# Kernel tuning notes

Hardware: AMD Instinct MI355X
Metric: run time of the kernel (lower is better)

Reference implementation:

```python
import jax, jax.numpy as jnp
import numpy as np


def setup_inputs() -> dict:
    key = jax.random.key(0)
    ks = jax.random.split(key, 8)
    B, N, C, H = 4, 1024, 512, 8
    return {
        "x": jax.random.normal(ks[0], (B, N, C), jnp.float32),
        "pos": jax.random.normal(ks[1], (B, N, 3), jnp.float32),
        "w_qkv": jax.random.normal(ks[2], (C, 3 * C), jnp.float32) * 0.02,
        "b_qkv": jax.random.normal(ks[3], (3 * C,), jnp.float32) * 0.02,
        "w1": jax.random.normal(ks[4], (3, 64), jnp.float32) * 0.1,
        "b1": jax.random.normal(ks[5], (64,), jnp.float32) * 0.1,
        "w2": jax.random.normal(ks[6], (64, H), jnp.float32) * 0.1,
        "b2": jax.random.normal(ks[7], (H,), jnp.float32) * 0.1,
    }


def reference(x, pos, w_qkv, b_qkv, w1, b1, w2, b2):
    B, N, C = x.shape
    H = w2.shape[1]          # num_heads
    D = C // H               # head_dim
    scale = D ** (-0.5)

    # qkv projection -> q, k, v each [B, H, N, D]
    qkv = (x @ w_qkv + b_qkv).reshape(B, N, 3, H, D)
    qkv = jnp.transpose(qkv, (2, 0, 3, 1, 4))
    q, k, v = qkv[0], qkv[1], qkv[2]

    # pairwise unit direction vectors [B, N, N, 3]
    pos_diff = pos[:, :, None, :] - pos[:, None, :, :]
    pos_norm = jnp.linalg.norm(pos_diff, axis=-1, keepdims=True) + 1e-6
    pos_dir = pos_diff / pos_norm

    # position-MLP bias: [B, N, N, H] -> [B, H, N, N]
    h = jax.nn.relu(pos_dir @ w1 + b1)
    bias = jnp.transpose(h @ w2 + b2, (0, 3, 1, 2))

    attn = jnp.einsum("bhnd,bhmd->bhnm", q, k) * scale + bias
    attn = jax.nn.softmax(attn, axis=-1)
    out = jnp.einsum("bhnm,bhmd->bhnd", attn, v)
    return jnp.transpose(out, (0, 2, 1, 3)).reshape(B, N, C)
```

## Files before the change

kernel.cpp:

```cpp
#include <hip/hip_runtime.h>
#include <hip/hip_bf16.h>
#include <math.h>


typedef __attribute__((ext_vector_type(8))) short bh8;
typedef __attribute__((ext_vector_type(4))) float f32x4;

static __device__ __forceinline__ ushort f2bf(float x) {
    __hip_bfloat16 h = __float2bfloat16(x);
    return *reinterpret_cast<ushort*>(&h);
}
static __device__ __forceinline__ float bf2f(ushort u) {
    unsigned v = ((unsigned)u) << 16;
    return __builtin_bit_cast(float, v);
}

__global__ __launch_bounds__(256) void pos_w1_kernel(
    const float* __restrict__ pos, const float* __restrict__ w1,
    float* __restrict__ apos)
{
    const int idx = blockIdx.x * 256 + threadIdx.x;
    const int bn = idx >> 6, j = idx & 63;
    const float px = pos[bn * 3 + 0];
    const float py = pos[bn * 3 + 1];
    const float pz = pos[bn * 3 + 2];
    apos[idx] = fmaf(px, w1[j], fmaf(py, w1[64 + j], pz * w1[128 + j]));
}

__global__ __launch_bounds__(256) void cast_x_split(
    const float* __restrict__ x, ushort* __restrict__ xh, ushort* __restrict__ xl)
{
    const int idx = blockIdx.x * 256 + threadIdx.x;
    const float4 v = *(const float4*)&x[(size_t)idx * 4];
    ushort h0 = f2bf(v.x), h1 = f2bf(v.y), h2 = f2bf(v.z), h3 = f2bf(v.w);
    ushort l0 = f2bf(v.x - bf2f(h0)), l1 = f2bf(v.y - bf2f(h1));
    ushort l2 = f2bf(v.z - bf2f(h2)), l3 = f2bf(v.w - bf2f(h3));
    uint2 hu, lu;
    hu.x = (unsigned)h0 | ((unsigned)h1 << 16);
    hu.y = (unsigned)h2 | ((unsigned)h3 << 16);
    lu.x = (unsigned)l0 | ((unsigned)l1 << 16);
    lu.y = (unsigned)l2 | ((unsigned)l3 << 16);
    *(uint2*)&xh[(size_t)idx * 4] = hu;
    *(uint2*)&xl[(size_t)idx * 4] = lu;
}

__global__ __launch_bounds__(256) void cast_wT_split(
    const float* __restrict__ w, ushort* __restrict__ wTh, ushort* __restrict__ wTl)
{
    __shared__ float t[64][65];
    const int n0 = blockIdx.x * 64;
    const int k0 = blockIdx.y * 64;
    const int tid = threadIdx.x;
    const int c = tid & 63, r4 = tid >> 6;
#pragma unroll
    for (int i = 0; i < 16; ++i) {
        const int r = i * 4 + r4;
        t[r][c] = w[(size_t)(k0 + r) * 1536 + n0 + c];
    }
    __syncthreads();
#pragma unroll
    for (int i = 0; i < 16; ++i) {
        const int r = i * 4 + r4;
        const float v = t[c][r];
        const ushort hv = f2bf(v);
        wTh[(size_t)(n0 + r) * 512 + k0 + c] = hv;
        wTl[(size_t)(n0 + r) * 512 + k0 + c] = f2bf(v - bf2f(hv));
    }
}

__global__ __launch_bounds__(256, 2) void qkv_mfma(
    const ushort* __restrict__ xh, const ushort* __restrict__ xl,
    const ushort* __restrict__ wTh, const ushort* __restrict__ wTl,
    const float* __restrict__ bqkv,
    ushort* __restrict__ qb, ushort* __restrict__ kb, ushort* __restrict__ vTb)
{
    __shared__ ushort Ah[128 * 68], Al[128 * 68], Bh[128 * 68], Bl[128 * 68];
    const int tid = threadIdx.x;
    const int m0 = blockIdx.x * 128;
    const int n0 = blockIdx.y * 128;
    const int wid = tid >> 6, lane = tid & 63;
    const int wr = wid >> 1, wc = wid & 1;
    const int lq = lane & 15, g = lane >> 4;

    f32x4 acc[4][4];
#pragma unroll
    for (int m = 0; m < 4; ++m)
#pragma unroll
        for (int n = 0; n < 4; ++n) acc[m][n] = (f32x4){0.f, 0.f, 0.f, 0.f};

    const int srow = tid >> 3;
    const int sc8 = (tid & 7) * 8;

    for (int kt = 0; kt < 8; ++kt) {
        const int kk0 = kt * 64;
        __syncthreads();
#pragma unroll
        for (int i = 0; i < 4; ++i) {
            const int row = i * 32 + srow;
            *(bh8*)&Ah[row * 68 + sc8] =
                *(const bh8*)&xh[(size_t)(m0 + row) * 512 + kk0 + sc8];
            *(bh8*)&Al[row * 68 + sc8] =
                *(const bh8*)&xl[(size_t)(m0 + row) * 512 + kk0 + sc8];
            *(bh8*)&Bh[row * 68 + sc8] =
                *(const bh8*)&wTh[(size_t)(n0 + row) * 512 + kk0 + sc8];
            *(bh8*)&Bl[row * 68 + sc8] =
                *(const bh8*)&wTl[(size_t)(n0 + row) * 512 + kk0 + sc8];
        }
        __syncthreads();
#pragma unroll
        for (int kc = 0; kc < 2; ++kc) {
            const int ko = kc * 32 + g * 8;
            bh8 afh[4], afl[4], bfh[4], bfl[4];
#pragma unroll
            for (int m = 0; m < 4; ++m) {
                afh[m] = *(const bh8*)&Ah[(wr * 64 + m * 16 + lq) * 68 + ko];
                afl[m] = *(const bh8*)&Al[(wr * 64 + m * 16 + lq) * 68 + ko];
            }
#pragma unroll
            for (int n = 0; n < 4; ++n) {
                bfh[n] = *(const bh8*)&Bh[(wc * 64 + n * 16 + lq) * 68 + ko];
                bfl[n] = *(const bh8*)&Bl[(wc * 64 + n * 16 + lq) * 68 + ko];
            }
#pragma unroll
            for (int m = 0; m < 4; ++m)
#pragma unroll
                for (int n = 0; n < 4; ++n) {
                    acc[m][n] = __builtin_amdgcn_mfma_f32_16x16x32_bf16(
                        afh[m], bfh[n], acc[m][n], 0, 0, 0);
                    acc[m][n] = __builtin_amdgcn_mfma_f32_16x16x32_bf16(
                        afh[m], bfl[n], acc[m][n], 0, 0, 0);
                    acc[m][n] = __builtin_amdgcn_mfma_f32_16x16x32_bf16(
                        afl[m], bfh[n], acc[m][n], 0, 0, 0);
                }
        }
    }

    const int s = n0 >> 9;
    const int rowB = m0 + wr * 64;
    const int b = rowB >> 10;
#pragma unroll
    for (int nt = 0; nt < 4; ++nt) {
        const int col = n0 + wc * 64 + nt * 16 + lq;
        const float bias_v = bqkv[col];
        const int h = (col >> 6) & 7, d = col & 63;
#pragma unroll
        for (int mt = 0; mt < 4; ++mt) {
            const int nloc = (rowB & 1023) + mt * 16 + g * 4;
            const float v0 = acc[mt][nt][0] + bias_v;
            const float v1 = acc[mt][nt][1] + bias_v;
            const float v2 = acc[mt][nt][2] + bias_v;
            const float v3 = acc[mt][nt][3] + bias_v;
            if (s == 0) {
                const size_t base = ((size_t)(b * 8 + h) * 1024 + nloc) * 64 + d;
                qb[base]       = f2bf(v0 * 0.125f);
                qb[base + 64]  = f2bf(v1 * 0.125f);
                qb[base + 128] = f2bf(v2 * 0.125f);
                qb[base + 192] = f2bf(v3 * 0.125f);
            } else if (s == 1) {
                const size_t base = ((size_t)(b * 8 + h) * 1024 + nloc) * 64 + d;
                kb[base]       = f2bf(v0);
                kb[base + 64]  = f2bf(v1);
                kb[base + 128] = f2bf(v2);
                kb[base + 192] = f2bf(v3);
            } else {
                uint2 u;
                u.x = (unsigned)f2bf(v0) | ((unsigned)f2bf(v1) << 16);
                u.y = (unsigned)f2bf(v2) | ((unsigned)f2bf(v3) << 16);
                *(uint2*)&vTb[((size_t)(b * 8 + h) * 64 + d) * 1024 + nloc] = u;
            }
        }
    }
}

__global__ __launch_bounds__(512, 4) void attn_fused(
    const ushort* __restrict__ qb, const ushort* __restrict__ kb,
    const ushort* __restrict__ vTb, const float* __restrict__ apos,
    const float* __restrict__ pos, const float* __restrict__ b1,
    const float* __restrict__ w2, const float* __restrict__ b2,
    float* __restrict__ outp0, float* __restrict__ outp1,
    float* __restrict__ ml0, float* __restrict__ ml1)
{
    const int bx = blockIdx.x;
    const int xcd = bx & 7;
    const int b = xcd >> 1;
    const int u = (bx >> 3) * 2 + (xcd & 1);
    const int nq0 = (u & 63) * 16;
    const int half = u >> 6;
    const int k0base = half * 512;

    float* __restrict__ outp = half ? outp1 : outp0;
    float* __restrict__ mlp  = half ? ml1 : ml0;

    const int tid = threadIdx.x;
    const int w = tid >> 6;
    const int lane = tid & 63;
    const int lq = lane & 15;
    const int g = lane >> 4;

    __shared__ __align__(16) float a_m_s[64][64];
    __shared__ __align__(16) float pos_k_s[64][4];
    __shared__ __align__(16) float bias_raw[8 * 1092 + 4];
    __shared__ __align__(16) ushort p_lds[8][16][72];
    __shared__ float red_s[8][20];

    float a_n[16], b1r[16];
    {
        const float* anp = apos + (size_t)(b * 1024 + nq0 + lq) * 64;
        *(float4*)&a_n[0]  = *(const float4*)&anp[g * 8];
        *(float4*)&a_n[4]  = *(const float4*)&anp[g * 8 + 4];
        *(float4*)&a_n[8]  = *(const float4*)&anp[32 + g * 8];
        *(float4*)&a_n[12] = *(const float4*)&anp[32 + g * 8 + 4];
        *(float4*)&b1r[0]  = *(const float4*)&b1[g * 8];
        *(float4*)&b1r[4]  = *(const float4*)&b1[g * 8 + 4];
        *(float4*)&b1r[8]  = *(const float4*)&b1[32 + g * 8];
        *(float4*)&b1r[12] = *(const float4*)&b1[32 + g * 8 + 4];
    }
    const float px = pos[(size_t)(b * 1024 + nq0 + lq) * 3 + 0];
    const float py = pos[(size_t)(b * 1024 + nq0 + lq) * 3 + 1];
    const float pz = pos[(size_t)(b * 1024 + nq0 + lq) * 3 + 2];

    bh8 w2fa, w2fb;
#pragma unroll
    for (int e = 0; e < 8; ++e) {
        const int k0 = g * 8 + e, k1 = 32 + g * 8 + e;
        w2fa[e] = (short)((lq < 8) ? f2bf(w2[k0 * 8 + lq]) : 0);
        w2fb[e] = (short)((lq < 8) ? f2bf(w2[k1 * 8 + lq]) : 0);
    }
    const float b2r = (lq < 8) ? b2[lq] : 0.f;

    bh8 qf0, qf1;
    {
        const ushort* qp = qb + ((size_t)(b * 8 + w) * 1024 + nq0 + lq) * 64;
        qf0 = *(const bh8*)&qp[g * 8];
        qf1 = *(const bh8*)&qp[32 + g * 8];
    }

    f32x4 o[4];
#pragma unroll
    for (int dt = 0; dt < 4; ++dt) o[dt] = (f32x4){0.f, 0.f, 0.f, 0.f};
    float m_run = -INFINITY, l_run = 0.f;

#define STAGE(m0v) do { \
        const float4* _src = (const float4*)(apos + (size_t)(b * 1024 + (m0v)) * 64); \
        float4* _dst = (float4*)&a_m_s[0][0]; \
        _dst[tid] = _src[tid]; \
        _dst[tid + 512] = _src[tid + 512]; \
        if (tid < 192) pos_k_s[tid / 3][tid % 3] = \
            pos[(size_t)(b * 1024 + (m0v) + tid / 3) * 3 + tid % 3]; \
    } while (0)

    STAGE(k0base);
    __syncthreads();

    for (int t16 = 0; t16 < 8; ++t16) {
        const int m0 = k0base + t16 * 64;

#pragma unroll
        for (int kk = 0; kk < 8; ++kk) {
            const int jl = w * 8 + kk;
            const float kx = pos_k_s[jl][0];
            const float ky = pos_k_s[jl][1];
            const float kz = pos_k_s[jl][2];
            const float dx = px - kx, dy = py - ky, dz = pz - kz;
            const float inv =
                1.f / (sqrtf(fmaf(dx, dx, fmaf(dy, dy, dz * dz))) + 1e-6f);
            const float* am = &a_m_s[jl][0];
            bh8 hf0, hf1;
#pragma unroll
            for (int e = 0; e < 8; ++e) {
                const float h0 =
                    fmaxf(fmaf(a_n[e] - am[g * 8 + e], inv, b1r[e]), 0.f);
                const float h1 =
                    fmaxf(fmaf(a_n[8 + e] - am[32 + g * 8 + e], inv, b1r[8 + e]), 0.f);
                hf0[e] = (short)f2bf(h0);
                hf1[e] = (short)f2bf(h1);
            }
            f32x4 acc = (f32x4){0.f, 0.f, 0.f, 0.f};
            acc = __builtin_amdgcn_mfma_f32_16x16x32_bf16(hf0, w2fa, acc, 0, 0, 0);
            acc = __builtin_amdgcn_mfma_f32_16x16x32_bf16(hf1, w2fb, acc, 0, 0, 0);
            if (lq < 8) {
#pragma unroll
                for (int r = 0; r < 4; ++r)
                    bias_raw[lq * 1092 + (g * 4 + r) * 68 + jl] = acc[r] + b2r;
            }
        }
        __syncthreads();

        if (t16 < 7) STAGE(m0 + 64);

        const ushort* kbp = kb + ((size_t)(b * 8 + w) * 1024 + m0) * 64;
        f32x4 s[4];
#pragma unroll
        for (int at = 0; at < 4; ++at) {
            const bh8 kf0 = *(const bh8*)&kbp[(at * 16 + lq) * 64 + g * 8];
            const bh8 kf1 = *(const bh8*)&kbp[(at * 16 + lq) * 64 + 32 + g * 8];
            f32x4 z = (f32x4){0.f, 0.f, 0.f, 0.f};
            z = __builtin_amdgcn_mfma_f32_16x16x32_bf16(kf0, qf0, z, 0, 0, 0);
            s[at] = __builtin_amdgcn_mfma_f32_16x16x32_bf16(kf1, qf1, z, 0, 0, 0);
        }

        float sv[16];
        float pmax = -INFINITY;
#pragma unroll
        for (int at = 0; at < 4; ++at) {
            const float4 bv = *(const float4*)
                &bias_raw[w * 1092 + lq * 68 + at * 16 + g * 4];
            sv[at * 4 + 0] = s[at][0] + bv.x;
            sv[at * 4 + 1] = s[at][1] + bv.y;
            sv[at * 4 + 2] = s[at][2] + bv.z;
            sv[at * 4 + 3] = s[at][3] + bv.w;
#pragma unroll
            for (int r = 0; r < 4; ++r) pmax = fmaxf(pmax, sv[at * 4 + r]);
        }
        pmax = fmaxf(pmax, __shfl_xor(pmax, 16));
        pmax = fmaxf(pmax, __shfl_xor(pmax, 32));
        const float mnew = fmaxf(m_run, pmax);
        const float alpha = __expf(m_run - mnew);
        m_run = mnew;

        float rs = 0.f;
        ushort pb[16];
#pragma unroll
        for (int i = 0; i < 16; ++i) {
            const float p = __expf(sv[i] - mnew);
            pb[i] = f2bf(p);
            rs += bf2f(pb[i]);
        }
        rs += __shfl_xor(rs, 16);
        rs += __shfl_xor(rs, 32);
        l_run = l_run * alpha + rs;

#pragma unroll
        for (int at = 0; at < 4; ++at) {
            uint2 uv;
            uv.x = (unsigned)pb[at * 4 + 0] | ((unsigned)pb[at * 4 + 1] << 16);
            uv.y = (unsigned)pb[at * 4 + 2] | ((unsigned)pb[at * 4 + 3] << 16);
            *(uint2*)&p_lds[w][lq][at * 16 + g * 4] = uv;
        }
        red_s[w][lq] = alpha;

        float ar[4];
#pragma unroll
        for (int r = 0; r < 4; ++r) ar[r] = red_s[w][g * 4 + r];
#pragma unroll
        for (int dt = 0; dt < 4; ++dt) {
            o[dt][0] *= ar[0]; o[dt][1] *= ar[1];
            o[dt][2] *= ar[2]; o[dt][3] *= ar[3];
        }

        const bh8 pa0 = *(const bh8*)&p_lds[w][lq][g * 8];
        const bh8 pa1 = *(const bh8*)&p_lds[w][lq][32 + g * 8];
        const ushort* vtp = vTb + ((size_t)(b * 8 + w) * 64) * 1024 + m0;
#pragma unroll
        for (int dt = 0; dt < 4; ++dt) {
            const bh8 vf0 = *(const bh8*)&vtp[(dt * 16 + lq) * 1024 + g * 8];
            const bh8 vf1 = *(const bh8*)&vtp[(dt * 16 + lq) * 1024 + 32 + g * 8];
            o[dt] = __builtin_amdgcn_mfma_f32_16x16x32_bf16(pa0, vf0, o[dt], 0, 0, 0);
            o[dt] = __builtin_amdgcn_mfma_f32_16x16x32_bf16(pa1, vf1, o[dt], 0, 0, 0);
        }
        __syncthreads();
    }

    if (g == 0) {
        float2 mlv;
        mlv.x = m_run;
        mlv.y = l_run;
        *(float2*)&mlp[((size_t)(b * 8 + w) * 1024 + nq0 + lq) * 2] = mlv;
    }
#pragma unroll
    for (int dt = 0; dt < 4; ++dt)
#pragma unroll
        for (int r = 0; r < 4; ++r)
            outp[(size_t)(b * 1024 + nq0 + g * 4 + r) * 512 + w * 64 + dt * 16 + lq] =
                o[dt][r];
#undef STAGE
}

__global__ __launch_bounds__(256) void combine_halves(
    const float* __restrict__ o0, const float* __restrict__ o1,
    const float* __restrict__ ml0, const float* __restrict__ ml1,
    float* __restrict__ outF)
{
    const int idx = blockIdx.x * 256 + threadIdx.x;
    const size_t c4 = (size_t)idx * 4;
    const int row = idx >> 7;
    const int coff = (idx & 127) * 4;
    const int h = coff >> 6;
    const int b = row >> 10, n = row & 1023;
    const size_t mli = ((size_t)(b * 8 + h) * 1024 + n) * 2;
    const float2 v0 = *(const float2*)&ml0[mli];
    const float2 v1 = *(const float2*)&ml1[mli];
    const float m = fmaxf(v0.x, v1.x);
    const float e0 = __expf(v0.x - m), e1 = __expf(v1.x - m);
    const float inv = 1.f / fmaf(v0.y, e0, v1.y * e1);
    const float4 a = *(const float4*)&o0[c4];
    const float4 bb = *(const float4*)&o1[c4];
    float4 r;
    r.x = fmaf(a.x, e0, bb.x * e1) * inv;
    r.y = fmaf(a.y, e0, bb.y * e1) * inv;
    r.z = fmaf(a.z, e0, bb.z * e1) * inv;
    r.w = fmaf(a.w, e0, bb.w * e1) * inv;
    *(float4*)&outF[c4] = r;
}

extern "C" void kernel_launch(void* const* d_in, const int* in_sizes, int n_in,
                              void* d_out, int out_size, void* d_ws, size_t ws_size,
                              hipStream_t stream) {
    const float* x    = (const float*)d_in[0];
    const float* pos  = (const float*)d_in[1];
    const float* wqkv = (const float*)d_in[2];
    const float* bqkv = (const float*)d_in[3];
    const float* w1   = (const float*)d_in[4];
    const float* b1   = (const float*)d_in[5];
    const float* w2   = (const float*)d_in[6];
    const float* b2   = (const float*)d_in[7];
    float* out = (float*)d_out;

    char* W = (char*)d_ws;
    ushort* qb    = (ushort*)W;
    ushort* kb    = (ushort*)(W + 4194304);
    ushort* vTb   = (ushort*)(W + 8388608);
    float*  apos  = (float*)(W + 12582912);
    ushort* xh    = (ushort*)(W + 13631488);
    ushort* xl    = (ushort*)(W + 17825792);
    float*  outp1 = (float*)(W + 13631488);
    ushort* wTh   = (ushort*)(W + 22020096);
    ushort* wTl   = (ushort*)(W + 23592960);
    float*  ml0   = (float*)(W + 22020096);
    float*  ml1   = (float*)(W + 22282240);
    float*  outp0 = out;

    hipLaunchKernelGGL(pos_w1_kernel, dim3(1024), dim3(256), 0, stream,
                       pos, w1, apos);
    hipLaunchKernelGGL(cast_x_split, dim3(2048), dim3(256), 0, stream,
                       x, xh, xl);
    hipLaunchKernelGGL(cast_wT_split, dim3(24, 8), dim3(256), 0, stream,
                       wqkv, wTh, wTl);
    hipLaunchKernelGGL(qkv_mfma, dim3(32, 12), dim3(256), 0, stream,
                       xh, xl, wTh, wTl, bqkv, qb, kb, vTb);
    hipLaunchKernelGGL(attn_fused, dim3(512), dim3(512), 0, stream,
                       qb, kb, vTb, apos, pos, b1, w2, b2,
                       outp0, outp1, ml0, ml1);
    hipLaunchKernelGGL(combine_halves, dim3(2048), dim3(256), 0, stream,
                       outp0, outp1, ml0, ml1, out);
}
```

Measured before the change: 204.4 us.

## Merge prep kernels, use exp2 softmax, fp16 bias in LDS, raise occupancy

Three preprocessing kernels are merged into one launch to cut launch overhead. The log2(e) factor is folded into the q scale and the position-MLP bias so softmax can use exp2f directly. The bias tile in LDS is stored as fp16 instead of fp32, halving its footprint, and the attention kernel's launch bound is raised from 4 to 6 blocks for more occupancy. The row sum now uses unrounded probabilities, and fp16 bias storage and tighter register limits could cost precision or cause spills.

```diff
diff --git a/kernel.cpp b/kernel.cpp
--- a/kernel.cpp
+++ b/kernel.cpp
@@ -1,10 +1,13 @@
 #include <hip/hip_runtime.h>
 #include <hip/hip_bf16.h>
+#include <hip/hip_fp16.h>
 #include <math.h>
 
 
 typedef __attribute__((ext_vector_type(8))) short bh8;
 typedef __attribute__((ext_vector_type(4))) float f32x4;
+
+#define LOG2E 1.44269504f
 
 static __device__ __forceinline__ ushort f2bf(float x) {
     __hip_bfloat16 h = __float2bfloat16(x);
@@ -14,57 +17,65 @@
     unsigned v = ((unsigned)u) << 16;
     return __builtin_bit_cast(float, v);
 }
-
-__global__ __launch_bounds__(256) void pos_w1_kernel(
-    const float* __restrict__ pos, const float* __restrict__ w1,
+static __device__ __forceinline__ ushort f2h(float x) {
+    __half h = __float2half(x);
+    return *reinterpret_cast<ushort*>(&h);
+}
+static __device__ __forceinline__ float h2f(ushort u) {
+    __half h = __builtin_bit_cast(__half, u);
+    return __half2float(h);
+}
+
+__global__ __launch_bounds__(256) void prep_kernel(
+    const float* __restrict__ x, const float* __restrict__ pos,
+    const float* __restrict__ w1, const float* __restrict__ wqkv,
+    ushort* __restrict__ xh, ushort* __restrict__ xl,
+    ushort* __restrict__ wTh, ushort* __restrict__ wTl,
     float* __restrict__ apos)
 {
-    const int idx = blockIdx.x * 256 + threadIdx.x;
-    const int bn = idx >> 6, j = idx & 63;
-    const float px = pos[bn * 3 + 0];
-    const float py = pos[bn * 3 + 1];
-    const float pz = pos[bn * 3 + 2];
-    apos[idx] = fmaf(px, w1[j], fmaf(py, w1[64 + j], pz * w1[128 + j]));
-}
-
-__global__ __launch_bounds__(256) void cast_x_split(
-    const float* __restrict__ x, ushort* __restrict__ xh, ushort* __restrict__ xl)
-{
-    const int idx = blockIdx.x * 256 + threadIdx.x;
-    const float4 v = *(const float4*)&x[(size_t)idx * 4];
-    ushort h0 = f2bf(v.x), h1 = f2bf(v.y), h2 = f2bf(v.z), h3 = f2bf(v.w);
-    ushort l0 = f2bf(v.x - bf2f(h0)), l1 = f2bf(v.y - bf2f(h1));
-    ushort l2 = f2bf(v.z - bf2f(h2)), l3 = f2bf(v.w - bf2f(h3));
-    uint2 hu, lu;
-    hu.x = (unsigned)h0 | ((unsigned)h1 << 16);
-    hu.y = (unsigned)h2 | ((unsigned)h3 << 16);
-    lu.x = (unsigned)l0 | ((unsigned)l1 << 16);
-    lu.y = (unsigned)l2 | ((unsigned)l3 << 16);
-    *(uint2*)&xh[(size_t)idx * 4] = hu;
-    *(uint2*)&xl[(size_t)idx * 4] = lu;
-}
-
-__global__ __launch_bounds__(256) void cast_wT_split(
-    const float* __restrict__ w, ushort* __restrict__ wTh, ushort* __restrict__ wTl)
-{
     __shared__ float t[64][65];
-    const int n0 = blockIdx.x * 64;
-    const int k0 = blockIdx.y * 64;
+    const int bid = blockIdx.x;
     const int tid = threadIdx.x;
-    const int c = tid & 63, r4 = tid >> 6;
-#pragma unroll
-    for (int i = 0; i < 16; ++i) {
-        const int r = i * 4 + r4;
-        t[r][c] = w[(size_t)(k0 + r) * 1536 + n0 + c];
-    }
-    __syncthreads();
-#pragma unroll
-    for (int i = 0; i < 16; ++i) {
-        const int r = i * 4 + r4;
-        const float v = t[c][r];
-        const ushort hv = f2bf(v);
-        wTh[(size_t)(n0 + r) * 512 + k0 + c] = hv;
-        wTl[(size_t)(n0 + r) * 512 + k0 + c] = f2bf(v - bf2f(hv));
+
+    if (bid < 2048) {
+        const int idx = bid * 256 + tid;
+        const float4 v = *(const float4*)&x[(size_t)idx * 4];
+        ushort h0 = f2bf(v.x), h1 = f2bf(v.y), h2 = f2bf(v.z), h3 = f2bf(v.w);
+        ushort l0 = f2bf(v.x - bf2f(h0)), l1 = f2bf(v.y - bf2f(h1));
+        ushort l2 = f2bf(v.z - bf2f(h2)), l3 = f2bf(v.w - bf2f(h3));
+        uint2 hu, lu;
+        hu.x = (unsigned)h0 | ((unsigned)h1 << 16);
+        hu.y = (unsigned)h2 | ((unsigned)h3 << 16);
+        lu.x = (unsigned)l0 | ((unsigned)l1 << 16);
+        lu.y = (unsigned)l2 | ((unsigned)l3 << 16);
+        *(uint2*)&xh[(size_t)idx * 4] = hu;
+        *(uint2*)&xl[(size_t)idx * 4] = lu;
+    } else if (bid < 3072) {
+        const int idx = (bid - 2048) * 256 + tid;
+        const int bn = idx >> 6, j = idx & 63;
+        const float px = pos[bn * 3 + 0];
+        const float py = pos[bn * 3 + 1];
+        const float pz = pos[bn * 3 + 2];
+        apos[idx] = fmaf(px, w1[j], fmaf(py, w1[64 + j], pz * w1[128 + j]));
+    } else {
+        const int tb = bid - 3072;
+        const int n0 = (tb % 24) * 64;
+        const int k0 = (tb / 24) * 64;
+        const int c = tid & 63, r4 = tid >> 6;
+#pragma unroll
+        for (int i = 0; i < 16; ++i) {
+            const int r = i * 4 + r4;
+            t[r][c] = wqkv[(size_t)(k0 + r) * 1536 + n0 + c];
+        }
+        __syncthreads();
+#pragma unroll
+        for (int i = 0; i < 16; ++i) {
+            const int r = i * 4 + r4;
+            const float v = t[c][r];
+            const ushort hv = f2bf(v);
+            wTh[(size_t)(n0 + r) * 512 + k0 + c] = hv;
+            wTl[(size_t)(n0 + r) * 512 + k0 + c] = f2bf(v - bf2f(hv));
+        }
     }
 }
 
@@ -138,6 +149,7 @@
     const int s = n0 >> 9;
     const int rowB = m0 + wr * 64;
     const int b = rowB >> 10;
+    const float QSCALE = 0.125f * LOG2E;
 #pragma unroll
     for (int nt = 0; nt < 4; ++nt) {
         const int col = n0 + wc * 64 + nt * 16 + lq;
@@ -152,10 +164,10 @@
             const float v3 = acc[mt][nt][3] + bias_v;
             if (s == 0) {
                 const size_t base = ((size_t)(b * 8 + h) * 1024 + nloc) * 64 + d;
-                qb[base]       = f2bf(v0 * 0.125f);
-                qb[base + 64]  = f2bf(v1 * 0.125f);
-                qb[base + 128] = f2bf(v2 * 0.125f);
-                qb[base + 192] = f2bf(v3 * 0.125f);
+                qb[base]       = f2bf(v0 * QSCALE);
+                qb[base + 64]  = f2bf(v1 * QSCALE);
+                qb[base + 128] = f2bf(v2 * QSCALE);
+                qb[base + 192] = f2bf(v3 * QSCALE);
             } else if (s == 1) {
                 const size_t base = ((size_t)(b * 8 + h) * 1024 + nloc) * 64 + d;
                 kb[base]       = f2bf(v0);
@@ -172,7 +184,7 @@
     }
 }
 
-__global__ __launch_bounds__(512, 4) void attn_fused(
+__global__ __launch_bounds__(512, 6) void attn_fused(
     const ushort* __restrict__ qb, const ushort* __restrict__ kb,
     const ushort* __restrict__ vTb, const float* __restrict__ apos,
     const float* __restrict__ pos, const float* __restrict__ b1,
@@ -199,9 +211,9 @@
 
     __shared__ __align__(16) float a_m_s[64][64];
     __shared__ __align__(16) float pos_k_s[64][4];
-    __shared__ __align__(16) float bias_raw[8 * 1092 + 4];
+    __shared__ __align__(16) ushort bias_s[8 * 1100];
     __shared__ __align__(16) ushort p_lds[8][16][72];
-    __shared__ float red_s[8][20];
+    __shared__ float red_s[8][18];
 
     float a_n[16], b1r[16];
     {
@@ -223,10 +235,10 @@
 #pragma unroll
     for (int e = 0; e < 8; ++e) {
         const int k0 = g * 8 + e, k1 = 32 + g * 8 + e;
-        w2fa[e] = (short)((lq < 8) ? f2bf(w2[k0 * 8 + lq]) : 0);
-        w2fb[e] = (short)((lq < 8) ? f2bf(w2[k1 * 8 + lq]) : 0);
-    }
-    const float b2r = (lq < 8) ? b2[lq] : 0.f;
+        w2fa[e] = (short)((lq < 8) ? f2bf(w2[k0 * 8 + lq] * LOG2E) : 0);
+        w2fb[e] = (short)((lq < 8) ? f2bf(w2[k1 * 8 + lq] * LOG2E) : 0);
+    }
+    const float b2r = (lq < 8) ? b2[lq] * LOG2E : 0.f;
 
     bh8 qf0, qf1;
     {
@@ -281,7 +293,7 @@
             if (lq < 8) {
 #pragma unroll
                 for (int r = 0; r < 4; ++r)
-                    bias_raw[lq * 1092 + (g * 4 + r) * 68 + jl] = acc[r] + b2r;
+                    bias_s[lq * 1100 + (g * 4 + r) * 68 + jl] = f2h(acc[r] + b2r);
             }
         }
         __syncthreads();
@@ -303,28 +315,28 @@
         float pmax = -INFINITY;
 #pragma unroll
         for (int at = 0; at < 4; ++at) {
-            const float4 bv = *(const float4*)
-                &bias_raw[w * 1092 + lq * 68 + at * 16 + g * 4];
-            sv[at * 4 + 0] = s[at][0] + bv.x;
-            sv[at * 4 + 1] = s[at][1] + bv.y;
-            sv[at * 4 + 2] = s[at][2] + bv.z;
-            sv[at * 4 + 3] = s[at][3] + bv.w;
+            const int bb = w * 1100 + lq * 68 + at * 16 + g * 4;
+            const uint2 bu = *(const uint2*)&bias_s[bb];
+            sv[at * 4 + 0] = s[at][0] + h2f((ushort)(bu.x & 0xffff));
+            sv[at * 4 + 1] = s[at][1] + h2f((ushort)(bu.x >> 16));
+            sv[at * 4 + 2] = s[at][2] + h2f((ushort)(bu.y & 0xffff));
+            sv[at * 4 + 3] = s[at][3] + h2f((ushort)(bu.y >> 16));
 #pragma unroll
             for (int r = 0; r < 4; ++r) pmax = fmaxf(pmax, sv[at * 4 + r]);
         }
         pmax = fmaxf(pmax, __shfl_xor(pmax, 16));
         pmax = fmaxf(pmax, __shfl_xor(pmax, 32));
         const float mnew = fmaxf(m_run, pmax);
-        const float alpha = __expf(m_run - mnew);
+        const float alpha = exp2f(m_run - mnew);
         m_run = mnew;
 
         float rs = 0.f;
         ushort pb[16];
 #pragma unroll
         for (int i = 0; i < 16; ++i) {
-            const float p = __expf(sv[i] - mnew);
+            const float p = exp2f(sv[i] - mnew);
             pb[i] = f2bf(p);
-            rs += bf2f(pb[i]);
+            rs += p;
         }
         rs += __shfl_xor(rs, 16);
         rs += __shfl_xor(rs, 32);
@@ -391,7 +403,7 @@
     const float2 v0 = *(const float2*)&ml0[mli];
     const float2 v1 = *(const float2*)&ml1[mli];
     const float m = fmaxf(v0.x, v1.x);
-    const float e0 = __expf(v0.x - m), e1 = __expf(v1.x - m);
+    const float e0 = exp2f(v0.x - m), e1 = exp2f(v1.x - m);
     const float inv = 1.f / fmaf(v0.y, e0, v1.y * e1);
     const float4 a = *(const float4*)&o0[c4];
     const float4 bb = *(const float4*)&o1[c4];
@@ -430,12 +442,8 @@
     float*  ml1   = (float*)(W + 22282240);
     float*  outp0 = out;
 
-    hipLaunchKernelGGL(pos_w1_kernel, dim3(1024), dim3(256), 0, stream,
-                       pos, w1, apos);
-    hipLaunchKernelGGL(cast_x_split, dim3(2048), dim3(256), 0, stream,
-                       x, xh, xl);
-    hipLaunchKernelGGL(cast_wT_split, dim3(24, 8), dim3(256), 0, stream,
-                       wqkv, wTh, wTl);
+    hipLaunchKernelGGL(prep_kernel, dim3(3264), dim3(256), 0, stream,
+                       x, pos, w1, wqkv, xh, xl, wTh, wTl, apos);
     hipLaunchKernelGGL(qkv_mfma, dim3(32, 12), dim3(256), 0, stream,
                        xh, xl, wTh, wTl, bqkv, qb, kb, vTb);
     hipLaunchKernelGGL(attn_fused, dim3(512), dim3(512), 0, stream,
```

Result: slower. 254.9 us (+24.7%).
